# Kernel tuning notes

Hardware: AMD Instinct MI355X
Metric: run time of the kernel (lower is better)

## Reference

```python
import jax, jax.numpy as jnp
import numpy as np

DIM = 64
N_HOP = 2
N_MEM = 32
BATCH = 512
N_ENT = 200000
N_REL = 32
KGE_W = 0.01
L2_W = 1e-7
EPS = 1e-7  # BCE clamp for stability


def setup_inputs() -> dict:
    key = jax.random.key(0)
    ks = jax.random.split(key, 11)
    return {
        "items": jax.random.randint(ks[0], (BATCH,), 0, N_ENT),
        "labels": jax.random.randint(ks[1], (BATCH,), 0, 2),
        "memories_h": jax.random.randint(ks[2], (N_HOP, BATCH, N_MEM), 0, N_ENT),
        "memories_r": jax.random.randint(ks[3], (N_HOP, BATCH, N_MEM), 0, N_REL),
        "memories_t": jax.random.randint(ks[4], (N_HOP, BATCH, N_MEM), 0, N_ENT),
        "entity_emb": jax.random.normal(ks[5], (N_ENT, DIM), jnp.float32) * 0.1,
        "relation_emb": jax.random.normal(ks[6], (N_REL, DIM * DIM), jnp.float32) * 0.02,
        "gru_wih": jax.random.normal(ks[7], (3 * DIM, DIM), jnp.float32) * 0.1,
        "gru_whh": jax.random.normal(ks[8], (3 * DIM, DIM), jnp.float32) * 0.1,
        "gru_bih": jnp.zeros((3 * DIM,), jnp.float32),
        "gru_bhh": jnp.zeros((3 * DIM,), jnp.float32),
    }


def _gru_scan(x_seq, h0, wih, whh, bih, bhh):
    """PyTorch nn.GRU on a 2D input treats dim 0 as the sequence axis (unbatched).
    x_seq: [B, D] scanned over B; h0: [D]. Gate order: r, z, n."""
    def step(h, x):
        gi = wih @ x + bih          # [3D]
        gh = whh @ h + bhh          # [3D]
        ir, iz, inn = jnp.split(gi, 3)
        hr, hz, hn = jnp.split(gh, 3)
        r = jax.nn.sigmoid(ir + hr)
        z = jax.nn.sigmoid(iz + hz)
        n = jnp.tanh(inn + r * hn)
        h_new = (1.0 - z) * n + z * h
        return h_new, h_new
    h_final, ys = jax.lax.scan(step, h0, x_seq)
    return ys, h_final


def reference(items, labels, memories_h, memories_r, memories_t,
              entity_emb, relation_emb, gru_wih, gru_whh, gru_bih, gru_bhh):
    item_emb = entity_emb[items]                                # [B, D]
    h_emb = entity_emb[memories_h]                              # [H, B, M, D]
    t_emb = entity_emb[memories_t]                              # [H, B, M, D]
    r_flat = relation_emb[memories_r]                           # [H, B, M, D*D]
    r_emb = r_flat.reshape(N_HOP, BATCH, N_MEM, DIM, DIM)       # [H, B, M, D, D]

    h_state = jnp.zeros((DIM,), item_emb.dtype)
    o_sum = jnp.zeros_like(item_emb)
    for hop in range(N_HOP):
        Rh = jnp.einsum('bmij,bmj->bmi', r_emb[hop], h_emb[hop])   # [B, M, D]
        probs = jax.nn.softmax(jnp.einsum('bmi,bi->bm', Rh, item_emb), axis=1)
        o = jnp.einsum('bm,bmd->bd', probs, t_emb[hop])            # [B, D]
        # GRU recurrence over the batch axis (faithful to the 2D-input quirk)
        item_emb, h_state = _gru_scan(item_emb, h_state, gru_wih, gru_whh, gru_bih, gru_bhh)
        o_sum = o_sum + o  # using_all_hops=True -> sum of all hops

    scores = jax.nn.sigmoid(jnp.sum(item_emb * o_sum, axis=1))     # [B]

    # losses
    lbl = labels.astype(scores.dtype)
    s = jnp.clip(scores, EPS, 1.0 - EPS)
    base_loss = -jnp.mean(lbl * jnp.log(s) + (1.0 - lbl) * jnp.log1p(-s))

    hRt = jnp.einsum('hbmi,hbmij,hbmj->hbm', h_emb, r_emb, t_emb)  # [H, B, M]
    kge_loss = -KGE_W * jnp.sum(jnp.mean(jax.nn.sigmoid(hRt), axis=(1, 2)))

    l2_loss = L2_W * (jnp.sum(h_emb * h_emb) + jnp.sum(t_emb * t_emb) + jnp.sum(r_flat * r_flat))

    loss = base_loss + kge_loss + l2_loss
    return scores, base_loss, kge_loss, l2_loss, loss
```

## Files before the change

### kernel.cpp

```cpp
#include <hip/hip_runtime.h>

#define DIM   64
#define G3    192
#define NB    512
#define NM    32
#define NRELS 32
#define KGE_W 0.01f
#define L2_W  1e-7f
#define EPSC  1e-7f


__device__ inline float bcast(float v, int srclane) {
    return __int_as_float(__builtin_amdgcn_readlane(__float_as_int(v), srclane));
}

__device__ inline float sigmoidf_(float x) { return 1.0f / (1.0f + __expf(-x)); }
__device__ inline float tanhf_(float x)    { return 1.0f - 2.0f / (1.0f + __expf(2.0f * x)); }

__device__ inline float wave_sum(float v) {
#pragma unroll
    for (int off = 32; off > 0; off >>= 1) v += __shfl_xor(v, off, 64);
    return v;
}
__device__ inline float wave_max(float v) {
#pragma unroll
    for (int off = 32; off > 0; off >>= 1) v = fmaxf(v, __shfl_xor(v, off, 64));
    return v;
}


__device__ void gru_scan(const float* __restrict__ GI,
                         const float* __restrict__ whh,
                         const float* __restrict__ bhh,
                         const float* __restrict__ h0,
                         float* __restrict__ ys,
                         float* __restrict__ hfin_out)
{
    const int lane = threadIdx.x & 63;

    float wr[DIM], wz[DIM], wn[DIM];
    {
        const float4* r4 = (const float4*)(whh + (0 * DIM + lane) * DIM);
        const float4* z4 = (const float4*)(whh + (1 * DIM + lane) * DIM);
        const float4* n4 = (const float4*)(whh + (2 * DIM + lane) * DIM);
#pragma unroll
        for (int i = 0; i < 16; ++i) {
            float4 a = r4[i]; wr[4*i] = a.x; wr[4*i+1] = a.y; wr[4*i+2] = a.z; wr[4*i+3] = a.w;
            float4 b = z4[i]; wz[4*i] = b.x; wz[4*i+1] = b.y; wz[4*i+2] = b.z; wz[4*i+3] = b.w;
            float4 c = n4[i]; wn[4*i] = c.x; wn[4*i+1] = c.y; wn[4*i+2] = c.z; wn[4*i+3] = c.w;
        }
    }
    const float br = bhh[lane], bz = bhh[DIM + lane], bn = bhh[2 * DIM + lane];

    float h = h0 ? h0[lane] : 0.0f;

    float c0 = GI[lane], c1 = GI[DIM + lane], c2 = GI[2 * DIM + lane];

    for (int t = 0; t < NB; ++t) {
        const int tn = (t + 1 < NB) ? t + 1 : NB - 1;
        const float* gp = GI + tn * G3;
        float p0 = gp[lane], p1 = gp[DIM + lane], p2 = gp[2 * DIM + lane];

        float ar0 = 0.f, ar1 = 0.f, ar2 = 0.f, ar3 = 0.f;
        float az0 = 0.f, az1 = 0.f, az2 = 0.f, az3 = 0.f;
        float an0 = 0.f, an1 = 0.f, an2 = 0.f, an3 = 0.f;
#pragma unroll
        for (int k = 0; k < 16; ++k) {
            float hk = bcast(h, k);
            ar0 = fmaf(wr[k], hk, ar0); az0 = fmaf(wz[k], hk, az0); an0 = fmaf(wn[k], hk, an0);
        }
#pragma unroll
        for (int k = 16; k < 32; ++k) {
            float hk = bcast(h, k);
            ar1 = fmaf(wr[k], hk, ar1); az1 = fmaf(wz[k], hk, az1); an1 = fmaf(wn[k], hk, an1);
        }
#pragma unroll
        for (int k = 32; k < 48; ++k) {
            float hk = bcast(h, k);
            ar2 = fmaf(wr[k], hk, ar2); az2 = fmaf(wz[k], hk, az2); an2 = fmaf(wn[k], hk, an2);
        }
#pragma unroll
        for (int k = 48; k < 64; ++k) {
            float hk = bcast(h, k);
            ar3 = fmaf(wr[k], hk, ar3); az3 = fmaf(wz[k], hk, az3); an3 = fmaf(wn[k], hk, an3);
        }
        float ghr = ((ar0 + ar1) + (ar2 + ar3)) + br;
        float ghz = ((az0 + az1) + (az2 + az3)) + bz;
        float ghn = ((an0 + an1) + (an2 + an3)) + bn;

        float r = sigmoidf_(c0 + ghr);
        float z = sigmoidf_(c1 + ghz);
        float n = tanhf_(c2 + r * ghn);
        h = n + z * (h - n);

        ys[t * DIM + lane] = h;
        c0 = p0; c1 = p1; c2 = p2;
    }
    if (hfin_out) hfin_out[lane] = h;
}


__global__ __launch_bounds__(64) void gi_kernel(const float* __restrict__ xsrc,
                                                const int* __restrict__ idx,
                                                const float* __restrict__ wih,
                                                const float* __restrict__ bih,
                                                const float* __restrict__ Rel,
                                                float* __restrict__ GI,
                                                float* __restrict__ relnorm)
{
    const int blk = blockIdx.x, lane = threadIdx.x;
    if (blk >= NB) {
        const int r = blk - NB;
        const float* R = Rel + r * DIM * DIM;
        float a = 0.0f;
#pragma unroll 4
        for (int i = 0; i < DIM; ++i) { float v = R[i * DIM + lane]; a = fmaf(v, v, a); }
        a = wave_sum(a);
        if (lane == 0) relnorm[r] = a;
        return;
    }
    const int b = blk;
    float xv = idx ? xsrc[idx[b] * DIM + lane] : xsrc[b * DIM + lane];
    float a0 = bih[lane], a1 = bih[DIM + lane], a2 = bih[2 * DIM + lane];
    const float* w0 = wih + (0 * DIM + lane) * DIM;
    const float* w1 = wih + (1 * DIM + lane) * DIM;
    const float* w2 = wih + (2 * DIM + lane) * DIM;
#pragma unroll 4
    for (int k = 0; k < DIM; ++k) {
        float xk = bcast(xv, k);
        a0 = fmaf(w0[k], xk, a0);
        a1 = fmaf(w1[k], xk, a1);
        a2 = fmaf(w2[k], xk, a2);
    }
    float* gp = GI + b * G3;
    gp[lane] = a0; gp[DIM + lane] = a1; gp[2 * DIM + lane] = a2;
}


__global__ __launch_bounds__(256, 1) void fused0(const float* __restrict__ E,
                                              const float* __restrict__ Rel,
                                              const int* __restrict__ items,
                                              const int* __restrict__ mh,
                                              const int* __restrict__ mr,
                                              const int* __restrict__ mt,
                                              const float* __restrict__ GI,
                                              const float* __restrict__ whh,
                                              const float* __restrict__ bhh,
                                              const float* __restrict__ relnorm,
                                              float* __restrict__ ys0,
                                              float* __restrict__ hfin,
                                              float* __restrict__ o0,
                                              float* __restrict__ kge_part,
                                              float* __restrict__ l2_part)
{
    if (blockIdx.x == 0) {
        if (threadIdx.x < 64) gru_scan(GI, whh, bhh, nullptr, ys0, hfin);
        return;
    }

    const int b = blockIdx.x - 1;
    const int tid = threadIdx.x, lane = tid & 63, wave = tid >> 6;
    __shared__ float logits[NM], probs[NM], opart[4][DIM], wred[4][4];

    float iv = E[items[b] * DIM + lane];
    float kge0 = 0.0f, kge1 = 0.0f, l2acc = 0.0f, r2acc = 0.0f;

    for (int mm = 0; mm < 8; ++mm) {
        const int m = wave * 8 + mm;
        const int base = b * NM + m;
        const int hidx = mh[base], ridx = mr[base], tidx = mt[base];
        float hv = E[hidx * DIM + lane];
        float tv = E[tidx * DIM + lane];
        l2acc = fmaf(hv, hv, l2acc);
        l2acc = fmaf(tv, tv, l2acc);
        r2acc += relnorm[ridx];
        const float* R = Rel + ridx * DIM * DIM;
        float accA = 0.0f, accK = 0.0f;
#pragma unroll 4
        for (int i = 0; i < DIM; ++i) {
            float rv = R[i * DIM + lane];
            accA = fmaf(bcast(iv, i), rv, accA);
            accK = fmaf(bcast(hv, i), rv, accK);
        }
        float la = wave_sum(accA * hv);
        float lk = wave_sum(accK * tv);
        if (lane == 0) logits[m] = la;
        kge0 += sigmoidf_(lk);
    }
    for (int mm = 0; mm < 8; ++mm) {
        const int m = wave * 8 + mm;
        const int base = NB * NM + b * NM + m;
        const int hidx = mh[base], ridx = mr[base], tidx = mt[base];
        float hv = E[hidx * DIM + lane];
        float tv = E[tidx * DIM + lane];
        l2acc = fmaf(hv, hv, l2acc);
        l2acc = fmaf(tv, tv, l2acc);
        r2acc += relnorm[ridx];
        const float* R = Rel + ridx * DIM * DIM;
        float accK = 0.0f;
#pragma unroll 4
        for (int i = 0; i < DIM; ++i)
            accK = fmaf(bcast(hv, i), R[i * DIM + lane], accK);
        kge1 += sigmoidf_(wave_sum(accK * tv));
    }
    __syncthreads();

    if (wave == 0) {
        float v = (lane < NM) ? logits[lane] : -1e30f;
        float mx = wave_max(v);
        float e = (lane < NM) ? __expf(v - mx) : 0.0f;
        float ssum = wave_sum(e);
        if (lane < NM) probs[lane] = e / ssum;
    }
    __syncthreads();

    float od = 0.0f;
    for (int mm = 0; mm < 8; ++mm) {
        const int m = wave * 8 + mm;
        const int tidx = mt[b * NM + m];
        od = fmaf(probs[m], E[tidx * DIM + lane], od);
    }
    opart[wave][lane] = od;
    float l2tot = wave_sum(l2acc);
    if (lane == 0) { wred[wave][0] = kge0; wred[wave][1] = kge1; wred[wave][2] = l2tot + r2acc; }
    __syncthreads();
    if (wave == 0)
        o0[b * DIM + lane] = opart[0][lane] + opart[1][lane] + opart[2][lane] + opart[3][lane];
    if (tid == 0) {
        kge_part[b * 2 + 0] = wred[0][0] + wred[1][0] + wred[2][0] + wred[3][0];
        kge_part[b * 2 + 1] = wred[0][1] + wred[1][1] + wred[2][1] + wred[3][1];
        l2_part[b]          = wred[0][2] + wred[1][2] + wred[2][2] + wred[3][2];
    }
}


__global__ __launch_bounds__(256, 1) void fused1(const float* __restrict__ E,
                                              const float* __restrict__ Rel,
                                              const int* __restrict__ mh,
                                              const int* __restrict__ mr,
                                              const int* __restrict__ mt,
                                              const float* __restrict__ GI,
                                              const float* __restrict__ whh,
                                              const float* __restrict__ bhh,
                                              const float* __restrict__ hfin,
                                              const float* __restrict__ ys0,
                                              float* __restrict__ ys1,
                                              const float* __restrict__ o0,
                                              float* __restrict__ osum)
{
    if (blockIdx.x == 0) {
        if (threadIdx.x < 64) gru_scan(GI, whh, bhh, hfin, ys1, nullptr);
        return;
    }

    const int b = blockIdx.x - 1;
    const int tid = threadIdx.x, lane = tid & 63, wave = tid >> 6;
    __shared__ float logits[NM], probs[NM], opart[4][DIM];

    float iv = ys0[b * DIM + lane];

    for (int mm = 0; mm < 8; ++mm) {
        const int m = wave * 8 + mm;
        const int base = NB * NM + b * NM + m;
        const int hidx = mh[base], ridx = mr[base];
        float hv = E[hidx * DIM + lane];
        const float* R = Rel + ridx * DIM * DIM;
        float accA = 0.0f;
#pragma unroll 4
        for (int i = 0; i < DIM; ++i)
            accA = fmaf(bcast(iv, i), R[i * DIM + lane], accA);
        float la = wave_sum(accA * hv);
        if (lane == 0) logits[m] = la;
    }
    __syncthreads();
    if (wave == 0) {
        float v = (lane < NM) ? logits[lane] : -1e30f;
        float mx = wave_max(v);
        float e = (lane < NM) ? __expf(v - mx) : 0.0f;
        float ssum = wave_sum(e);
        if (lane < NM) probs[lane] = e / ssum;
    }
    __syncthreads();
    float od = 0.0f;
    for (int mm = 0; mm < 8; ++mm) {
        const int m = wave * 8 + mm;
        const int tidx = mt[NB * NM + b * NM + m];
        od = fmaf(probs[m], E[tidx * DIM + lane], od);
    }
    opart[wave][lane] = od;
    __syncthreads();
    if (wave == 0)
        osum[b * DIM + lane] = o0[b * DIM + lane] +
            opart[0][lane] + opart[1][lane] + opart[2][lane] + opart[3][lane];
}


__global__ __launch_bounds__(512) void finalize(const float* __restrict__ ys1,
                                                const float* __restrict__ osum,
                                                const int* __restrict__ labels,
                                                const float* __restrict__ kge_part,
                                                const float* __restrict__ l2_part,
                                                float* __restrict__ out)
{
    __shared__ float red[512];
    const int tid = threadIdx.x;

    float dot = 0.0f;
    const float* a = ys1 + tid * DIM;
    const float* c = osum + tid * DIM;
#pragma unroll 8
    for (int k = 0; k < DIM; ++k) dot = fmaf(a[k], c[k], dot);
    float score = sigmoidf_(dot);
    out[tid] = score;

    float s = fminf(fmaxf(score, EPSC), 1.0f - EPSC);
    float term = labels[tid] ? logf(s) : log1pf(-s);

    float bsum, ksum, lsum;
    {
        red[tid] = term; __syncthreads();
#pragma unroll
        for (int st = 256; st > 0; st >>= 1) { if (tid < st) red[tid] += red[tid + st]; __syncthreads(); }
        bsum = red[0]; __syncthreads();
    }
    {
        red[tid] = kge_part[2 * tid] + kge_part[2 * tid + 1]; __syncthreads();
#pragma unroll
        for (int st = 256; st > 0; st >>= 1) { if (tid < st) red[tid] += red[tid + st]; __syncthreads(); }
        ksum = red[0]; __syncthreads();
    }
    {
        red[tid] = l2_part[tid]; __syncthreads();
#pragma unroll
        for (int st = 256; st > 0; st >>= 1) { if (tid < st) red[tid] += red[tid + st]; __syncthreads(); }
        lsum = red[0];
    }

    if (tid == 0) {
        float base = -bsum / (float)NB;
        float kge  = -KGE_W * ksum / (float)(NB * NM);
        float l2   = L2_W * lsum;
        out[NB + 0] = base;
        out[NB + 1] = kge;
        out[NB + 2] = l2;
        out[NB + 3] = base + kge + l2;
    }
}


extern "C" void kernel_launch(void* const* d_in, const int* in_sizes, int n_in,
                              void* d_out, int out_size, void* d_ws, size_t ws_size,
                              hipStream_t stream) {
    const int*   items  = (const int*)d_in[0];
    const int*   labels = (const int*)d_in[1];
    const int*   mh     = (const int*)d_in[2];
    const int*   mr     = (const int*)d_in[3];
    const int*   mt     = (const int*)d_in[4];
    const float* E      = (const float*)d_in[5];
    const float* Rel    = (const float*)d_in[6];
    const float* wih    = (const float*)d_in[7];
    const float* whh    = (const float*)d_in[8];
    const float* bih    = (const float*)d_in[9];
    const float* bhh    = (const float*)d_in[10];
    float* out = (float*)d_out;
    float* ws  = (float*)d_ws;

    float* GI      = ws;
    float* ys0     = GI + 98304;
    float* ys1     = ys0 + 32768;
    float* hfin    = ys1 + 32768;
    float* o0      = hfin + 64;
    float* osum    = o0 + 32768;
    float* relnorm = osum + 32768;
    float* kge_p   = relnorm + 32;
    float* l2_p    = kge_p + 1024;

    gi_kernel<<<NB + NRELS, 64, 0, stream>>>(E, items, wih, bih, Rel, GI, relnorm);
    fused0<<<NB + 1, 256, 0, stream>>>(E, Rel, items, mh, mr, mt, GI, whh, bhh,
                                       relnorm, ys0, hfin, o0, kge_p, l2_p);
    gi_kernel<<<NB, 64, 0, stream>>>(ys0, nullptr, wih, bih, Rel, GI, relnorm);
    fused1<<<NB + 1, 256, 0, stream>>>(E, Rel, mh, mr, mt, GI, whh, bhh, hfin,
                                       ys0, ys1, o0, osum);
    finalize<<<1, 512, 0, stream>>>(ys1, osum, labels, kge_p, l2_p, out);
}
```

Measured before the change: 541.0 us.

## Split GRU scan out of fused attention kernels into separate launches

Separates the single-wave GRU recurrence from the per-batch attention kernels into its own kernel, launched after each attention kernel, and uses separate GI buffers per hop. Attention kernels drop the minimum-blocks launch bound, which may allow more occupancy. The cost is losing the overlap between the sequential GRU scan and the attention work, which puts the scan latency on the critical path twice.

```diff
diff --git a/kernel.cpp b/kernel.cpp
--- a/kernel.cpp
+++ b/kernel.cpp
@@ -29,12 +29,12 @@
 }
 
 
-__device__ void gru_scan(const float* __restrict__ GI,
-                         const float* __restrict__ whh,
-                         const float* __restrict__ bhh,
-                         const float* __restrict__ h0,
-                         float* __restrict__ ys,
-                         float* __restrict__ hfin_out)
+__global__ __launch_bounds__(64, 1) void gru_kernel(const float* __restrict__ GI,
+                                                    const float* __restrict__ whh,
+                                                    const float* __restrict__ bhh,
+                                                    const float* __restrict__ h0,
+                                                    float* __restrict__ ys,
+                                                    float* __restrict__ hfin_out)
 {
     const int lane = threadIdx.x & 63;
 
@@ -137,28 +137,18 @@
 }
 
 
-__global__ __launch_bounds__(256, 1) void fused0(const float* __restrict__ E,
-                                              const float* __restrict__ Rel,
-                                              const int* __restrict__ items,
-                                              const int* __restrict__ mh,
-                                              const int* __restrict__ mr,
-                                              const int* __restrict__ mt,
-                                              const float* __restrict__ GI,
-                                              const float* __restrict__ whh,
-                                              const float* __restrict__ bhh,
-                                              const float* __restrict__ relnorm,
-                                              float* __restrict__ ys0,
-                                              float* __restrict__ hfin,
-                                              float* __restrict__ o0,
-                                              float* __restrict__ kge_part,
-                                              float* __restrict__ l2_part)
-{
-    if (blockIdx.x == 0) {
-        if (threadIdx.x < 64) gru_scan(GI, whh, bhh, nullptr, ys0, hfin);
-        return;
-    }
-
-    const int b = blockIdx.x - 1;
+__global__ __launch_bounds__(256) void att0(const float* __restrict__ E,
+                                            const float* __restrict__ Rel,
+                                            const int* __restrict__ items,
+                                            const int* __restrict__ mh,
+                                            const int* __restrict__ mr,
+                                            const int* __restrict__ mt,
+                                            const float* __restrict__ relnorm,
+                                            float* __restrict__ o0,
+                                            float* __restrict__ kge_part,
+                                            float* __restrict__ l2_part)
+{
+    const int b = blockIdx.x;
     const int tid = threadIdx.x, lane = tid & 63, wave = tid >> 6;
     __shared__ float logits[NM], probs[NM], opart[4][DIM], wred[4][4];
 
@@ -234,26 +224,16 @@
 }
 
 
-__global__ __launch_bounds__(256, 1) void fused1(const float* __restrict__ E,
-                                              const float* __restrict__ Rel,
-                                              const int* __restrict__ mh,
-                                              const int* __restrict__ mr,
-                                              const int* __restrict__ mt,
-                                              const float* __restrict__ GI,
-                                              const float* __restrict__ whh,
-                                              const float* __restrict__ bhh,
-                                              const float* __restrict__ hfin,
-                                              const float* __restrict__ ys0,
-                                              float* __restrict__ ys1,
-                                              const float* __restrict__ o0,
-                                              float* __restrict__ osum)
-{
-    if (blockIdx.x == 0) {
-        if (threadIdx.x < 64) gru_scan(GI, whh, bhh, hfin, ys1, nullptr);
-        return;
-    }
-
-    const int b = blockIdx.x - 1;
+__global__ __launch_bounds__(256) void att1(const float* __restrict__ E,
+                                            const float* __restrict__ Rel,
+                                            const int* __restrict__ mh,
+                                            const int* __restrict__ mr,
+                                            const int* __restrict__ mt,
+                                            const float* __restrict__ ys0,
+                                            const float* __restrict__ o0,
+                                            float* __restrict__ osum)
+{
+    const int b = blockIdx.x;
     const int tid = threadIdx.x, lane = tid & 63, wave = tid >> 6;
     __shared__ float logits[NM], probs[NM], opart[4][DIM];
 
@@ -365,8 +345,9 @@
     float* out = (float*)d_out;
     float* ws  = (float*)d_ws;
 
-    float* GI      = ws;
-    float* ys0     = GI + 98304;
+    float* GI0     = ws;
+    float* GI1     = GI0 + 98304;
+    float* ys0     = GI1 + 98304;
     float* ys1     = ys0 + 32768;
     float* hfin    = ys1 + 32768;
     float* o0      = hfin + 64;
@@ -375,11 +356,11 @@
     float* kge_p   = relnorm + 32;
     float* l2_p    = kge_p + 1024;
 
-    gi_kernel<<<NB + NRELS, 64, 0, stream>>>(E, items, wih, bih, Rel, GI, relnorm);
-    fused0<<<NB + 1, 256, 0, stream>>>(E, Rel, items, mh, mr, mt, GI, whh, bhh,
-                                       relnorm, ys0, hfin, o0, kge_p, l2_p);
-    gi_kernel<<<NB, 64, 0, stream>>>(ys0, nullptr, wih, bih, Rel, GI, relnorm);
-    fused1<<<NB + 1, 256, 0, stream>>>(E, Rel, mh, mr, mt, GI, whh, bhh, hfin,
-                                       ys0, ys1, o0, osum);
+    gi_kernel<<<NB + NRELS, 64, 0, stream>>>(E, items, wih, bih, Rel, GI0, relnorm);
+    att0<<<NB, 256, 0, stream>>>(E, Rel, items, mh, mr, mt, relnorm, o0, kge_p, l2_p);
+    gru_kernel<<<1, 64, 0, stream>>>(GI0, whh, bhh, nullptr, ys0, hfin);
+    gi_kernel<<<NB, 64, 0, stream>>>(ys0, nullptr, wih, bih, Rel, GI1, relnorm);
+    att1<<<NB, 256, 0, stream>>>(E, Rel, mh, mr, mt, ys0, o0, osum);
+    gru_kernel<<<1, 64, 0, stream>>>(GI1, whh, bhh, hfin, ys1, nullptr);
     finalize<<<1, 512, 0, stream>>>(ys1, osum, labels, kge_p, l2_p, out);
 }
```

Result: slower. 609.7 us (+12.7%).

## Double-buffer GRU input gates in LDS using producer waves during scan

Applied to the files above, without the earlier changes.

The serial GRU scan block now uses its three idle waves to stage the precomputed input-gate vectors into a double-buffered shared-memory tile, chunk by chunk, while wave 0 runs the recurrence out of LDS. This replaces per-step global loads on the latency-critical serial path with LDS reads. It also splits the GI workspace into separate buffers for each hop. The cost is a block-wide barrier every 32 steps and about 48KB of extra shared memory in both fused kernels, which may lower occupancy for the non-scan blocks.

```diff
diff --git a/kernel.cpp b/kernel.cpp
--- a/kernel.cpp
+++ b/kernel.cpp
@@ -5,6 +5,8 @@
 #define NB    512
 #define NM    32
 #define NRELS 32
+#define CH    32
+#define NCH   (NB/CH)
 #define KGE_W 0.01f
 #define L2_W  1e-7f
 #define EPSC  1e-7f
@@ -29,74 +31,98 @@
 }
 
 
-__device__ void gru_scan(const float* __restrict__ GI,
-                         const float* __restrict__ whh,
-                         const float* __restrict__ bhh,
-                         const float* __restrict__ h0,
-                         float* __restrict__ ys,
-                         float* __restrict__ hfin_out)
+__device__ __forceinline__ void gru_scan_staged(float (*gibuf)[CH * G3],
+                                                const float* __restrict__ GI,
+                                                const float* __restrict__ whh,
+                                                const float* __restrict__ bhh,
+                                                const float* __restrict__ h0,
+                                                float* __restrict__ ys,
+                                                float* __restrict__ hfin_out)
 {
-    const int lane = threadIdx.x & 63;
-
-    float wr[DIM], wz[DIM], wn[DIM];
-    {
-        const float4* r4 = (const float4*)(whh + (0 * DIM + lane) * DIM);
-        const float4* z4 = (const float4*)(whh + (1 * DIM + lane) * DIM);
-        const float4* n4 = (const float4*)(whh + (2 * DIM + lane) * DIM);
-#pragma unroll
-        for (int i = 0; i < 16; ++i) {
-            float4 a = r4[i]; wr[4*i] = a.x; wr[4*i+1] = a.y; wr[4*i+2] = a.z; wr[4*i+3] = a.w;
-            float4 b = z4[i]; wz[4*i] = b.x; wz[4*i+1] = b.y; wz[4*i+2] = b.z; wz[4*i+3] = b.w;
-            float4 c = n4[i]; wn[4*i] = c.x; wn[4*i+1] = c.y; wn[4*i+2] = c.z; wn[4*i+3] = c.w;
+    const int tid  = threadIdx.x;
+    const int lane = tid & 63;
+    const int wave = tid >> 6;
+
+    if (wave != 0) {
+        const int sid = tid - 64;
+        const float4* src = (const float4*)GI;
+        float4* dst = (float4*)gibuf[0];
+#pragma unroll
+        for (int j = 0; j < 8; ++j) dst[sid + j * 192] = src[sid + j * 192];
+    }
+    __syncthreads();
+
+    if (wave == 0) {
+        float wr[DIM], wz[DIM], wn[DIM];
+        {
+            const float4* r4 = (const float4*)(whh + (0 * DIM + lane) * DIM);
+            const float4* z4 = (const float4*)(whh + (1 * DIM + lane) * DIM);
+            const float4* n4 = (const float4*)(whh + (2 * DIM + lane) * DIM);
+#pragma unroll
+            for (int i = 0; i < 16; ++i) {
+                float4 a = r4[i]; wr[4*i] = a.x; wr[4*i+1] = a.y; wr[4*i+2] = a.z; wr[4*i+3] = a.w;
+                float4 b = z4[i]; wz[4*i] = b.x; wz[4*i+1] = b.y; wz[4*i+2] = b.z; wz[4*i+3] = b.w;
+                float4 c = n4[i]; wn[4*i] = c.x; wn[4*i+1] = c.y; wn[4*i+2] = c.z; wn[4*i+3] = c.w;
+            }
         }
-    }
-    const float br = bhh[lane], bz = bhh[DIM + lane], bn = bhh[2 * DIM + lane];
-
-    float h = h0 ? h0[lane] : 0.0f;
-
-    float c0 = GI[lane], c1 = GI[DIM + lane], c2 = GI[2 * DIM + lane];
-
-    for (int t = 0; t < NB; ++t) {
-        const int tn = (t + 1 < NB) ? t + 1 : NB - 1;
-        const float* gp = GI + tn * G3;
-        float p0 = gp[lane], p1 = gp[DIM + lane], p2 = gp[2 * DIM + lane];
-
-        float ar0 = 0.f, ar1 = 0.f, ar2 = 0.f, ar3 = 0.f;
-        float az0 = 0.f, az1 = 0.f, az2 = 0.f, az3 = 0.f;
-        float an0 = 0.f, an1 = 0.f, an2 = 0.f, an3 = 0.f;
-#pragma unroll
-        for (int k = 0; k < 16; ++k) {
-            float hk = bcast(h, k);
-            ar0 = fmaf(wr[k], hk, ar0); az0 = fmaf(wz[k], hk, az0); an0 = fmaf(wn[k], hk, an0);
+        const float br = bhh[lane], bz = bhh[DIM + lane], bn = bhh[2 * DIM + lane];
+        float h = h0 ? h0[lane] : 0.0f;
+
+        for (int c = 0; c < NCH; ++c) {
+            const float* buf = gibuf[c & 1];
+            for (int tl = 0; tl < CH; ++tl) {
+                const float* gi = buf + tl * G3;
+                float c0 = gi[lane], c1 = gi[DIM + lane], c2 = gi[2 * DIM + lane];
+
+                float ar0 = 0.f, ar1 = 0.f, ar2 = 0.f, ar3 = 0.f;
+                float az0 = 0.f, az1 = 0.f, az2 = 0.f, az3 = 0.f;
+                float an0 = 0.f, an1 = 0.f, an2 = 0.f, an3 = 0.f;
+#pragma unroll
+                for (int k = 0; k < 16; ++k) {
+                    float hk = bcast(h, k);
+                    ar0 = fmaf(wr[k], hk, ar0); az0 = fmaf(wz[k], hk, az0); an0 = fmaf(wn[k], hk, an0);
+                }
+#pragma unroll
+                for (int k = 16; k < 32; ++k) {
+                    float hk = bcast(h, k);
+                    ar1 = fmaf(wr[k], hk, ar1); az1 = fmaf(wz[k], hk, az1); an1 = fmaf(wn[k], hk, an1);
+                }
+#pragma unroll
+                for (int k = 32; k < 48; ++k) {
+                    float hk = bcast(h, k);
+                    ar2 = fmaf(wr[k], hk, ar2); az2 = fmaf(wz[k], hk, az2); an2 = fmaf(wn[k], hk, an2);
+                }
+#pragma unroll
+                for (int k = 48; k < 64; ++k) {
+                    float hk = bcast(h, k);
+                    ar3 = fmaf(wr[k], hk, ar3); az3 = fmaf(wz[k], hk, az3); an3 = fmaf(wn[k], hk, an3);
+                }
+                float ghr = ((ar0 + ar1) + (ar2 + ar3)) + br;
+                float ghz = ((az0 + az1) + (az2 + az3)) + bz;
+                float ghn = ((an0 + an1) + (an2 + an3)) + bn;
+
+                float r = sigmoidf_(c0 + ghr);
+                float z = sigmoidf_(c1 + ghz);
+                float n = tanhf_(c2 + r * ghn);
+                h = n + z * (h - n);
+
+                ys[(c * CH + tl) * DIM + lane] = h;
+            }
+            __syncthreads();
         }
-#pragma unroll
-        for (int k = 16; k < 32; ++k) {
-            float hk = bcast(h, k);
-            ar1 = fmaf(wr[k], hk, ar1); az1 = fmaf(wz[k], hk, az1); an1 = fmaf(wn[k], hk, an1);
+        if (hfin_out) hfin_out[lane] = h;
+    } else {
+        const int sid = tid - 64;
+        for (int c = 0; c < NCH; ++c) {
+            if (c + 1 < NCH) {
+                const float4* src = (const float4*)(GI + (size_t)(c + 1) * CH * G3);
+                float4* dst = (float4*)gibuf[(c + 1) & 1];
+#pragma unroll
+                for (int j = 0; j < 8; ++j) dst[sid + j * 192] = src[sid + j * 192];
+            }
+            __syncthreads();
         }
-#pragma unroll
-        for (int k = 32; k < 48; ++k) {
-            float hk = bcast(h, k);
-            ar2 = fmaf(wr[k], hk, ar2); az2 = fmaf(wz[k], hk, az2); an2 = fmaf(wn[k], hk, an2);
-        }
-#pragma unroll
-        for (int k = 48; k < 64; ++k) {
-            float hk = bcast(h, k);
-            ar3 = fmaf(wr[k], hk, ar3); az3 = fmaf(wz[k], hk, az3); an3 = fmaf(wn[k], hk, an3);
-        }
-        float ghr = ((ar0 + ar1) + (ar2 + ar3)) + br;
-        float ghz = ((az0 + az1) + (az2 + az3)) + bz;
-        float ghn = ((an0 + an1) + (an2 + an3)) + bn;
-
-        float r = sigmoidf_(c0 + ghr);
-        float z = sigmoidf_(c1 + ghz);
-        float n = tanhf_(c2 + r * ghn);
-        h = n + z * (h - n);
-
-        ys[t * DIM + lane] = h;
-        c0 = p0; c1 = p1; c2 = p2;
-    }
-    if (hfin_out) hfin_out[lane] = h;
+    }
 }
 
 
@@ -153,14 +179,16 @@
                                               float* __restrict__ kge_part,
                                               float* __restrict__ l2_part)
 {
+    __shared__ __align__(16) float gibuf[2][CH * G3];
+    __shared__ float logits[NM], probs[NM], opart[4][DIM], wred[4][4];
+
     if (blockIdx.x == 0) {
-        if (threadIdx.x < 64) gru_scan(GI, whh, bhh, nullptr, ys0, hfin);
+        gru_scan_staged(gibuf, GI, whh, bhh, nullptr, ys0, hfin);
         return;
     }
 
     const int b = blockIdx.x - 1;
     const int tid = threadIdx.x, lane = tid & 63, wave = tid >> 6;
-    __shared__ float logits[NM], probs[NM], opart[4][DIM], wred[4][4];
 
     float iv = E[items[b] * DIM + lane];
     float kge0 = 0.0f, kge1 = 0.0f, l2acc = 0.0f, r2acc = 0.0f;
@@ -248,14 +276,16 @@
                                               const float* __restrict__ o0,
                                               float* __restrict__ osum)
 {
+    __shared__ __align__(16) float gibuf[2][CH * G3];
+    __shared__ float logits[NM], probs[NM], opart[4][DIM];
+
     if (blockIdx.x == 0) {
-        if (threadIdx.x < 64) gru_scan(GI, whh, bhh, hfin, ys1, nullptr);
+        gru_scan_staged(gibuf, GI, whh, bhh, hfin, ys1, nullptr);
         return;
     }
 
     const int b = blockIdx.x - 1;
     const int tid = threadIdx.x, lane = tid & 63, wave = tid >> 6;
-    __shared__ float logits[NM], probs[NM], opart[4][DIM];
 
     float iv = ys0[b * DIM + lane];
 
@@ -365,8 +395,9 @@
     float* out = (float*)d_out;
     float* ws  = (float*)d_ws;
 
-    float* GI      = ws;
-    float* ys0     = GI + 98304;
+    float* GI0     = ws;
+    float* GI1     = GI0 + 98304;
+    float* ys0     = GI1 + 98304;
     float* ys1     = ys0 + 32768;
     float* hfin    = ys1 + 32768;
     float* o0      = hfin + 64;
@@ -375,11 +406,11 @@
     float* kge_p   = relnorm + 32;
     float* l2_p    = kge_p + 1024;
 
-    gi_kernel<<<NB + NRELS, 64, 0, stream>>>(E, items, wih, bih, Rel, GI, relnorm);
-    fused0<<<NB + 1, 256, 0, stream>>>(E, Rel, items, mh, mr, mt, GI, whh, bhh,
+    gi_kernel<<<NB + NRELS, 64, 0, stream>>>(E, items, wih, bih, Rel, GI0, relnorm);
+    fused0<<<NB + 1, 256, 0, stream>>>(E, Rel, items, mh, mr, mt, GI0, whh, bhh,
                                        relnorm, ys0, hfin, o0, kge_p, l2_p);
-    gi_kernel<<<NB, 64, 0, stream>>>(ys0, nullptr, wih, bih, Rel, GI, relnorm);
-    fused1<<<NB + 1, 256, 0, stream>>>(E, Rel, mh, mr, mt, GI, whh, bhh, hfin,
+    gi_kernel<<<NB, 64, 0, stream>>>(ys0, nullptr, wih, bih, Rel, GI1, relnorm);
+    fused1<<<NB + 1, 256, 0, stream>>>(E, Rel, mh, mr, mt, GI1, whh, bhh, hfin,
                                        ys0, ys1, o0, osum);
     finalize<<<1, 512, 0, stream>>>(ys1, osum, labels, kge_p, l2_p, out);
 }
```

After: 531.9 us. About the same (-1.7%).
